# Kernel optimization log

Measured on AMD Instinct MI355X. Metric: run time of the kernel, lower is better.

## Reference

```python
import jax, jax.numpy as jnp
import numpy as np

D_MODEL = 1024
NUM_HEADS = 16
D_K = D_MODEL // NUM_HEADS


def setup_inputs() -> dict:
    key = jax.random.key(0)
    ks = jax.random.split(key, 11)
    B, S = 2, 2048
    scale = 1.0 / np.sqrt(D_MODEL)
    inp = {
        "Q": jax.random.normal(ks[0], (B, S, D_MODEL), jnp.float32),
        "K": jax.random.normal(ks[1], (B, S, D_MODEL), jnp.float32),
        "V": jax.random.normal(ks[2], (B, S, D_MODEL), jnp.float32),
        "W_q": jax.random.normal(ks[3], (D_MODEL, D_MODEL), jnp.float32) * scale,
        "b_q": jnp.zeros((D_MODEL,), jnp.float32),
        "W_k": jax.random.normal(ks[4], (D_MODEL, D_MODEL), jnp.float32) * scale,
        "b_k": jnp.zeros((D_MODEL,), jnp.float32),
        "W_v": jax.random.normal(ks[5], (D_MODEL, D_MODEL), jnp.float32) * scale,
        "b_v": jnp.zeros((D_MODEL,), jnp.float32),
        "W_o": jax.random.normal(ks[6], (D_MODEL, D_MODEL), jnp.float32) * scale,
        "b_o": jnp.zeros((D_MODEL,), jnp.float32),
    }
    return inp


def _split_heads(x):
    B, S, _ = x.shape
    return x.reshape(B, S, NUM_HEADS, D_K).transpose(0, 2, 1, 3)  # [B,H,S,dk]


def reference(Q, K, V, W_q, b_q, W_k, b_k, W_v, b_v, W_o, b_o):
    # Linear projections (torch Linear: x @ W^T + b)
    q = _split_heads(Q @ W_q.T + b_q)
    k = _split_heads(K @ W_k.T + b_k)
    v = _split_heads(V @ W_v.T + b_v)
    scale = 1.0 / jnp.sqrt(jnp.float32(D_K))
    scores = jnp.einsum("bhqd,bhkd->bhqk", q, k) * scale  # [B,H,S,S]
    attn = jax.nn.softmax(scores, axis=-1)
    # dropout is identity in eval mode
    out = jnp.einsum("bhqk,bhkd->bhqd", attn, v)  # [B,H,S,dk]
    B, H, S, dk = out.shape
    out = out.transpose(0, 2, 1, 3).reshape(B, S, H * dk)
    output = out @ W_o.T + b_o
    return output, attn
```

## Files before the change

### kernel.cpp

```cpp
#include <hip/hip_runtime.h>

typedef __bf16 bf16x8 __attribute__((ext_vector_type(8)));
typedef float f32x4 __attribute__((ext_vector_type(4)));
typedef unsigned short u16x4 __attribute__((ext_vector_type(4)));
typedef unsigned short u16x8 __attribute__((ext_vector_type(8)));

#define DEV __device__ __forceinline__

DEV unsigned short f2bf(float x) {
    union { float f; unsigned u; } v; v.f = x;
    unsigned r = (v.u + 0x7FFFu + ((v.u >> 16) & 1u)) >> 16;
    return (unsigned short)r;
}
DEV float bf2f(unsigned short h) {
    union { unsigned u; float f; } v; v.u = ((unsigned)h) << 16;
    return v.f;
}
DEV void gload16(const void* g, void* l) {
    __builtin_amdgcn_global_load_lds((const __attribute__((address_space(1))) void*)g,
                                     (__attribute__((address_space(3))) void*)l, 16, 0, 0);
}

__global__ __launch_bounds__(512) void gemm_proj(
    const float* __restrict__ A0, const float* __restrict__ A1, const float* __restrict__ A2,
    const float* __restrict__ W0, const float* __restrict__ W1, const float* __restrict__ W2,
    const float* __restrict__ B0, const float* __restrict__ B1, const float* __restrict__ B2,
    unsigned short* O0, unsigned short* O1, unsigned short* O2)
{
    const int raw = blockIdx.x;
    const int f = (raw & 7) * 48 + (raw >> 3);
    const int bx = f % 8;
    const int by = (f / 8) % 16;
    const int z  = f / 128;

    const float* A       = (z == 0) ? A0 : (z == 1) ? A1 : A2;
    const float* W       = (z == 0) ? W0 : (z == 1) ? W1 : W2;
    const float* bias    = (z == 0) ? B0 : (z == 1) ? B1 : B2;
    unsigned short* outp = (z == 0) ? O0 : (z == 1) ? O1 : O2;

    __shared__ unsigned short sA[256 * 32];
    __shared__ unsigned short sB[128 * 32];

    const int tid = threadIdx.x, lane = tid & 63;
    const int wv = tid >> 6, wrow = wv >> 2, wcol = wv & 3;
    const int l15 = lane & 15, lg = lane >> 4;
    const int row0 = by * 256, col0 = bx * 128;

    f32x4 acc[8][2];
#pragma unroll
    for (int m = 0; m < 8; ++m)
#pragma unroll
        for (int n = 0; n < 2; ++n) acc[m][n] = f32x4{0.f, 0.f, 0.f, 0.f};

    const int rA = tid >> 1, cA = (tid & 1) * 16;
    const int rB = tid >> 2, cB = (tid & 3) * 8;
    const float* Abase = A + (size_t)(row0 + rA) * 1024 + cA;
    const float* Wbase = W + (size_t)(col0 + rB) * 1024 + cB;

    for (int kt = 0; kt < 32; ++kt) {
        const int kf = kt * 32;
        f32x4 a0 = *(const f32x4*)(Abase + kf);
        f32x4 a1 = *(const f32x4*)(Abase + kf + 4);
        f32x4 a2 = *(const f32x4*)(Abase + kf + 8);
        f32x4 a3 = *(const f32x4*)(Abase + kf + 12);
        f32x4 w0 = *(const f32x4*)(Wbase + kf);
        f32x4 w1 = *(const f32x4*)(Wbase + kf + 4);
        u16x8 pa0, pa1, pw;
#pragma unroll
        for (int j = 0; j < 4; ++j) {
            pa0[j] = f2bf(a0[j]); pa0[4 + j] = f2bf(a1[j]);
            pa1[j] = f2bf(a2[j]); pa1[4 + j] = f2bf(a3[j]);
            pw[j]  = f2bf(w0[j]); pw[4 + j]  = f2bf(w1[j]);
        }
        __syncthreads();
        *(u16x8*)&sA[rA * 32 + cA]     = pa0;
        *(u16x8*)&sA[rA * 32 + cA + 8] = pa1;
        *(u16x8*)&sB[rB * 32 + cB]     = pw;
        __syncthreads();

        bf16x8 af[8], bfr[2];
#pragma unroll
        for (int m = 0; m < 8; ++m) {
            int arow = wrow * 128 + m * 16 + l15;
            af[m] = *(const bf16x8*)&sA[arow * 32 + lg * 8];
        }
#pragma unroll
        for (int n = 0; n < 2; ++n) {
            int bcol = wcol * 32 + n * 16 + l15;
            bfr[n] = *(const bf16x8*)&sB[bcol * 32 + lg * 8];
        }
#pragma unroll
        for (int m = 0; m < 8; ++m)
#pragma unroll
            for (int n = 0; n < 2; ++n)
                acc[m][n] = __builtin_amdgcn_mfma_f32_16x16x32_bf16(af[m], bfr[n], acc[m][n], 0, 0, 0);
    }

#pragma unroll
    for (int m = 0; m < 8; ++m) {
#pragma unroll
        for (int n = 0; n < 2; ++n) {
            const int C = col0 + wcol * 32 + n * 16 + l15;
            const int Rbase = row0 + wrow * 128 + m * 16 + lg * 4;
            const float bv = bias[C];
            const int bq = Rbase >> 11, s0 = Rbase & 2047, hh = C >> 6, dd = C & 63;
            if (z != 2) {
                const size_t base = ((size_t)(bq * 16 + hh) * 2048 + s0) * 64 + dd;
#pragma unroll
                for (int j = 0; j < 4; ++j)
                    outp[base + (size_t)j * 64] = f2bf(acc[m][n][j] + bv);
            } else {
                const size_t base = ((size_t)(bq * 16 + hh) * 64 + dd) * 2048 + s0;
                u16x4 pk;
#pragma unroll
                for (int j = 0; j < 4; ++j) pk[j] = f2bf(acc[m][n][j] + bv);
                *(u16x4*)&outp[base] = pk;
            }
        }
    }
}

__global__ __launch_bounds__(256) void gemm_final(
    const unsigned short* __restrict__ A, const float* __restrict__ W,
    const float* __restrict__ bias, float* __restrict__ out)
{
    const int raw = blockIdx.x;
    const int f = (raw & 7) * 64 + (raw >> 3);
    const int bx = f % 16;
    const int by = f / 16;

    __shared__ unsigned short sA[128 * 32];
    __shared__ unsigned short sB[64 * 32];

    const int tid = threadIdx.x, lane = tid & 63;
    const int wv = tid >> 6, wrow = wv >> 1, wcol = wv & 1;
    const int l15 = lane & 15, lg = lane >> 4;
    const int row0 = by * 128, col0 = bx * 64;

    f32x4 acc[4][2];
#pragma unroll
    for (int m = 0; m < 4; ++m)
#pragma unroll
        for (int n = 0; n < 2; ++n) acc[m][n] = f32x4{0.f, 0.f, 0.f, 0.f};

    const char* Ab = (const char*)(A + (size_t)row0 * 1024);
    const int o1 = tid * 16, o2 = (256 + tid) * 16;
    const int r1 = o1 >> 6, c1 = o1 & 63, r2 = o2 >> 6, c2 = o2 & 63;
    const int rB = tid >> 2, cB = (tid & 3) * 8;
    const float* Wbase = W + (size_t)(col0 + rB) * 1024 + cB;

    for (int kt = 0; kt < 32; ++kt) {
        const int kb = kt * 64;
        f32x4 w0 = *(const f32x4*)(Wbase + kt * 32);
        f32x4 w1 = *(const f32x4*)(Wbase + kt * 32 + 4);
        u16x8 pw;
#pragma unroll
        for (int j = 0; j < 4; ++j) { pw[j] = f2bf(w0[j]); pw[4 + j] = f2bf(w1[j]); }
        __syncthreads();
        gload16(Ab + (size_t)r1 * 2048 + kb + c1, (char*)sA + o1);
        gload16(Ab + (size_t)r2 * 2048 + kb + c2, (char*)sA + o2);
        *(u16x8*)&sB[rB * 32 + cB] = pw;
        __syncthreads();

        bf16x8 af[4], bfr[2];
#pragma unroll
        for (int m = 0; m < 4; ++m) {
            int arow = wrow * 64 + m * 16 + l15;
            af[m] = *(const bf16x8*)&sA[arow * 32 + lg * 8];
        }
#pragma unroll
        for (int n = 0; n < 2; ++n) {
            int bcol = wcol * 32 + n * 16 + l15;
            bfr[n] = *(const bf16x8*)&sB[bcol * 32 + lg * 8];
        }
#pragma unroll
        for (int m = 0; m < 4; ++m)
#pragma unroll
            for (int n = 0; n < 2; ++n)
                acc[m][n] = __builtin_amdgcn_mfma_f32_16x16x32_bf16(af[m], bfr[n], acc[m][n], 0, 0, 0);
    }

#pragma unroll
    for (int m = 0; m < 4; ++m) {
#pragma unroll
        for (int n = 0; n < 2; ++n) {
            const int C = col0 + wcol * 32 + n * 16 + l15;
            const int Rbase = row0 + wrow * 64 + m * 16 + lg * 4;
            const float bv = bias[C];
            const size_t base = (size_t)Rbase * 1024 + C;
#pragma unroll
            for (int j = 0; j < 4; ++j)
                __builtin_nontemporal_store(acc[m][n][j] + bv, &out[base + (size_t)j * 1024]);
        }
    }
}

__global__ __launch_bounds__(512, 1) void attn_k(
    const unsigned short* __restrict__ qh, const unsigned short* __restrict__ kh,
    const unsigned short* __restrict__ vT, unsigned short* __restrict__ oa,
    float* __restrict__ attn_out)
{
    __shared__ unsigned short p[32 * 2048];
    __shared__ float Olds[2][32][64];
    __shared__ float wsum[8][32];
    __shared__ float rinvw[8][32];

    const int tid = threadIdx.x, lane = tid & 63, w = tid >> 6;
    const int l15 = lane & 15, lg = lane >> 4;

    const int raw = blockIdx.x;
    const int f = (raw & 7) * 256 + (raw >> 3);
    const int q0 = (f & 63) * 32;
    const int h = (f >> 6) & 15, b = f >> 10;

    const size_t headoff = (size_t)(b * 16 + h) * 131072;
    const unsigned short* qhead = qh + headoff + (size_t)q0 * 64;
    const unsigned short* khead = kh + headoff;
    const unsigned short* vhead = vT + headoff;

    const int colbase = w * 256;
    const bf16x8 aq0 = *(const bf16x8*)(qhead + l15 * 64 + lg * 8);
    const bf16x8 aq1 = *(const bf16x8*)(qhead + l15 * 64 + 32 + lg * 8);
    const bf16x8 aq2 = *(const bf16x8*)(qhead + (16 + l15) * 64 + lg * 8);
    const bf16x8 aq3 = *(const bf16x8*)(qhead + (16 + l15) * 64 + 32 + lg * 8);

    const unsigned short* kptr = khead + (size_t)(colbase + l15) * 64 + lg * 8;
    bf16x8 kf0 = *(const bf16x8*)(kptr);
    bf16x8 kf1 = *(const bf16x8*)(kptr + 32);
    float psum0 = 0.f, psum1 = 0.f;

#pragma unroll
    for (int t = 0; t < 16; ++t) {
        bf16x8 nk0, nk1;
        if (t < 15) {
            const unsigned short* np = kptr + (size_t)(t + 1) * 1024;
            nk0 = *(const bf16x8*)(np);
            nk1 = *(const bf16x8*)(np + 32);
        }
        f32x4 c0 = {0.f, 0.f, 0.f, 0.f}, c1 = {0.f, 0.f, 0.f, 0.f};
        c0 = __builtin_amdgcn_mfma_f32_16x16x32_bf16(kf0, aq0, c0, 0, 0, 0);
        c1 = __builtin_amdgcn_mfma_f32_16x16x32_bf16(kf0, aq2, c1, 0, 0, 0);
        c0 = __builtin_amdgcn_mfma_f32_16x16x32_bf16(kf1, aq1, c0, 0, 0, 0);
        c1 = __builtin_amdgcn_mfma_f32_16x16x32_bf16(kf1, aq3, c1, 0, 0, 0);
        u16x4 pk0, pk1;
#pragma unroll
        for (int j = 0; j < 4; ++j) {
            float e0 = __expf(c0[j] * 0.125f);
            float e1 = __expf(c1[j] * 0.125f);
            psum0 += e0; psum1 += e1;
            pk0[j] = f2bf(e0); pk1[j] = f2bf(e1);
        }
        const int colb = (colbase + t * 16 + lg * 4) << 1;
        int b0 = (l15 << 12) + colb;         b0 ^= (l15 & 7) << 4;
        int b1 = ((16 + l15) << 12) + colb;  b1 ^= (l15 & 7) << 4;
        *(u16x4*)((char*)p + b0) = pk0;
        *(u16x4*)((char*)p + b1) = pk1;
        kf0 = nk0; kf1 = nk1;
    }

    psum0 += __shfl_xor(psum0, 16);
    psum0 += __shfl_xor(psum0, 32);
    psum1 += __shfl_xor(psum1, 16);
    psum1 += __shfl_xor(psum1, 32);
    if (lane < 16) {
        wsum[w][lane]      = psum0;
        wsum[w][16 + lane] = psum1;
    }
    __syncthreads();

    if (lane < 32) {
        float s = wsum[0][lane] + wsum[1][lane] + wsum[2][lane] + wsum[3][lane]
                + wsum[4][lane] + wsum[5][lane] + wsum[6][lane] + wsum[7][lane];
        rinvw[w][lane] = 1.0f / s;
    }

    float* aout = attn_out + ((size_t)(b * 16 + h) * 2048 + q0) * 2048;
    for (int i = 0; i < 32; ++i) {
        int byte = (i << 12) + (tid << 3);
        byte ^= (i & 7) << 4;
        const u16x4 pv = *(const u16x4*)((char*)p + byte);
        const float inv = rinvw[w][i];
        f32x4 ov = { bf2f(pv[0]) * inv, bf2f(pv[1]) * inv, bf2f(pv[2]) * inv, bf2f(pv[3]) * inv };
        __builtin_nontemporal_store(ov, (f32x4*)&aout[(size_t)i * 2048 + tid * 4]);
    }

    const int dq = w & 3, kh2 = w >> 2;
    const int d0 = dq * 16;
    f32x4 acc0 = {0.f, 0.f, 0.f, 0.f}, acc1 = {0.f, 0.f, 0.f, 0.f};
    const unsigned short* vptr = vhead + (size_t)(d0 + l15) * 2048 + kh2 * 1024 + lg * 8;
    bf16x8 vf = *(const bf16x8*)(vptr);
    for (int kc = 0; kc < 32; ++kc) {
        bf16x8 nvf;
        if (kc < 31) nvf = *(const bf16x8*)(vptr + (size_t)(kc + 1) * 32);
        const int colb = (kh2 * 1024 + kc * 32 + lg * 8) << 1;
        int b0 = (l15 << 12) + colb;         b0 ^= (l15 & 7) << 4;
        int b1 = ((16 + l15) << 12) + colb;  b1 ^= (l15 & 7) << 4;
        const bf16x8 pa0 = *(const bf16x8*)((char*)p + b0);
        const bf16x8 pa1 = *(const bf16x8*)((char*)p + b1);
        acc0 = __builtin_amdgcn_mfma_f32_16x16x32_bf16(pa0, vf, acc0, 0, 0, 0);
        acc1 = __builtin_amdgcn_mfma_f32_16x16x32_bf16(pa1, vf, acc1, 0, 0, 0);
        vf = nvf;
    }
#pragma unroll
    for (int j = 0; j < 4; ++j) {
        Olds[kh2][lg * 4 + j][d0 + l15]      = acc0[j];
        Olds[kh2][16 + lg * 4 + j][d0 + l15] = acc1[j];
    }
    __syncthreads();

    {
        const int q = tid >> 4, d4 = (tid & 15) * 4;
        f32x4 s = *(const f32x4*)&Olds[0][q][d4];
        s += *(const f32x4*)&Olds[1][q][d4];
        const float rq = rinvw[w][q];
        u16x4 pk;
#pragma unroll
        for (int j = 0; j < 4; ++j) pk[j] = f2bf(s[j] * rq);
        *(u16x4*)&oa[((size_t)b * 2048 + q0 + q) * 1024 + h * 64 + d4] = pk;
    }
}

extern "C" void kernel_launch(void* const* d_in, const int* in_sizes, int n_in,
                              void* d_out, int out_size, void* d_ws, size_t ws_size,
                              hipStream_t stream) {
    const float* Q  = (const float*)d_in[0];
    const float* K  = (const float*)d_in[1];
    const float* V  = (const float*)d_in[2];
    const float* Wq = (const float*)d_in[3];
    const float* bq = (const float*)d_in[4];
    const float* Wk = (const float*)d_in[5];
    const float* bk = (const float*)d_in[6];
    const float* Wv = (const float*)d_in[7];
    const float* bv = (const float*)d_in[8];
    const float* Wo = (const float*)d_in[9];
    const float* bo = (const float*)d_in[10];

    char* ws = (char*)d_ws;
    unsigned short* qhd = (unsigned short*)(ws + 33554432);
    unsigned short* khd = (unsigned short*)(ws + 41943040);
    unsigned short* vTd = (unsigned short*)(ws + 50331648);
    unsigned short* oad = (unsigned short*)(ws + 58720256);

    float* out = (float*)d_out;
    float* attn_out = out + 4194304;

    gemm_proj<<<dim3(384), 512, 0, stream>>>(Q, K, V, Wq, Wk, Wv,
                                             bq, bk, bv, qhd, khd, vTd);

    attn_k<<<dim3(2048), 512, 0, stream>>>(qhd, khd, vTd, oad, attn_out);

    gemm_final<<<dim3(512), 256, 0, stream>>>(oad, Wo, bo, out);
}
```

Measured before the change: 249.7 us.

## Fuse P·V into the score loop using register-held probabilities and permuted V layout

The projection kernel now writes transposed V with a permuted sequence order, so the bf16 probability fragments produced by the QK^T MFMAs can be fed directly as A operands of the P·V MFMAs without going back through LDS. Each wave accumulates its own partial output over its 256 key columns, and the partials from all 8 waves are reduced through LDS, reusing the probability buffer. This removes the separate P·V pass that re-read P from LDS and overlaps the V loads with the score computation. The costs are more registers, an 8-way instead of 2-way reduction, and an extra barrier; launch bounds were also changed to ask for 2 blocks per CU, though 128KB of shared memory probably still limits occupancy to one.

```diff
diff --git a/kernel.cpp b/kernel.cpp
--- a/kernel.cpp
+++ b/kernel.cpp
@@ -110,7 +110,8 @@
                 for (int j = 0; j < 4; ++j)
                     outp[base + (size_t)j * 64] = f2bf(acc[m][n][j] + bv);
             } else {
-                const size_t base = ((size_t)(bq * 16 + hh) * 64 + dd) * 2048 + s0;
+                const int sp = (s0 & ~31) + (((s0 >> 2) & 3) << 3) + (((s0 >> 4) & 1) << 2);
+                const size_t base = ((size_t)(bq * 16 + hh) * 64 + dd) * 2048 + sp;
                 u16x4 pk;
 #pragma unroll
                 for (int j = 0; j < 4; ++j) pk[j] = f2bf(acc[m][n][j] + bv);
@@ -195,13 +196,12 @@
     }
 }
 
-__global__ __launch_bounds__(512, 1) void attn_k(
+__global__ __launch_bounds__(512, 2) void attn_k(
     const unsigned short* __restrict__ qh, const unsigned short* __restrict__ kh,
     const unsigned short* __restrict__ vT, unsigned short* __restrict__ oa,
     float* __restrict__ attn_out)
 {
     __shared__ unsigned short p[32 * 2048];
-    __shared__ float Olds[2][32][64];
     __shared__ float wsum[8][32];
     __shared__ float rinvw[8][32];
 
@@ -225,9 +225,23 @@
     const bf16x8 aq3 = *(const bf16x8*)(qhead + (16 + l15) * 64 + 32 + lg * 8);
 
     const unsigned short* kptr = khead + (size_t)(colbase + l15) * 64 + lg * 8;
+    const unsigned short* vbase = vhead + (size_t)l15 * 2048 + colbase + lg * 8;
+
     bf16x8 kf0 = *(const bf16x8*)(kptr);
     bf16x8 kf1 = *(const bf16x8*)(kptr + 32);
+    bf16x8 vfc[4], vfn[4];
+#pragma unroll
+    for (int dq = 0; dq < 4; ++dq)
+        vfc[dq] = *(const bf16x8*)(vbase + (size_t)dq * 32768);
+
     float psum0 = 0.f, psum1 = 0.f;
+    f32x4 oacc[2][4];
+#pragma unroll
+    for (int qh2 = 0; qh2 < 2; ++qh2)
+#pragma unroll
+        for (int dq = 0; dq < 4; ++dq) oacc[qh2][dq] = f32x4{0.f, 0.f, 0.f, 0.f};
+
+    u16x4 pe0, pe1;
 
 #pragma unroll
     for (int t = 0; t < 16; ++t) {
@@ -237,6 +251,12 @@
             nk0 = *(const bf16x8*)(np);
             nk1 = *(const bf16x8*)(np + 32);
         }
+        if ((t & 1) == 0 && t < 14) {
+            const int nc = (t >> 1) + 1;
+#pragma unroll
+            for (int dq = 0; dq < 4; ++dq)
+                vfn[dq] = *(const bf16x8*)(vbase + (size_t)dq * 32768 + nc * 32);
+        }
         f32x4 c0 = {0.f, 0.f, 0.f, 0.f}, c1 = {0.f, 0.f, 0.f, 0.f};
         c0 = __builtin_amdgcn_mfma_f32_16x16x32_bf16(kf0, aq0, c0, 0, 0, 0);
         c1 = __builtin_amdgcn_mfma_f32_16x16x32_bf16(kf0, aq2, c1, 0, 0, 0);
@@ -250,11 +270,32 @@
             psum0 += e0; psum1 += e1;
             pk0[j] = f2bf(e0); pk1[j] = f2bf(e1);
         }
-        const int colb = (colbase + t * 16 + lg * 4) << 1;
-        int b0 = (l15 << 12) + colb;         b0 ^= (l15 & 7) << 4;
-        int b1 = ((16 + l15) << 12) + colb;  b1 ^= (l15 & 7) << 4;
-        *(u16x4*)((char*)p + b0) = pk0;
-        *(u16x4*)((char*)p + b1) = pk1;
+        {
+            const int colb = (colbase + t * 16 + lg * 4) << 1;
+            int b0 = (l15 << 12) + colb;         b0 ^= (l15 & 7) << 4;
+            int b1 = ((16 + l15) << 12) + colb;  b1 ^= (l15 & 7) << 4;
+            *(u16x4*)((char*)p + b0) = pk0;
+            *(u16x4*)((char*)p + b1) = pk1;
+        }
+        if ((t & 1) == 0) {
+            pe0 = pk0; pe1 = pk1;
+        } else {
+            u16x8 a0v, a1v;
+#pragma unroll
+            for (int j = 0; j < 4; ++j) {
+                a0v[j] = pe0[j]; a0v[4 + j] = pk0[j];
+                a1v[j] = pe1[j]; a1v[4 + j] = pk1[j];
+            }
+            const bf16x8 a0 = __builtin_bit_cast(bf16x8, a0v);
+            const bf16x8 a1 = __builtin_bit_cast(bf16x8, a1v);
+#pragma unroll
+            for (int dq = 0; dq < 4; ++dq) {
+                oacc[0][dq] = __builtin_amdgcn_mfma_f32_16x16x32_bf16(a0, vfc[dq], oacc[0][dq], 0, 0, 0);
+                oacc[1][dq] = __builtin_amdgcn_mfma_f32_16x16x32_bf16(a1, vfc[dq], oacc[1][dq], 0, 0, 0);
+            }
+#pragma unroll
+            for (int dq = 0; dq < 4; ++dq) vfc[dq] = vfn[dq];
+        }
         kf0 = nk0; kf1 = nk1;
     }
 
@@ -283,35 +324,24 @@
         f32x4 ov = { bf2f(pv[0]) * inv, bf2f(pv[1]) * inv, bf2f(pv[2]) * inv, bf2f(pv[3]) * inv };
         __builtin_nontemporal_store(ov, (f32x4*)&aout[(size_t)i * 2048 + tid * 4]);
     }
-
-    const int dq = w & 3, kh2 = w >> 2;
-    const int d0 = dq * 16;
-    f32x4 acc0 = {0.f, 0.f, 0.f, 0.f}, acc1 = {0.f, 0.f, 0.f, 0.f};
-    const unsigned short* vptr = vhead + (size_t)(d0 + l15) * 2048 + kh2 * 1024 + lg * 8;
-    bf16x8 vf = *(const bf16x8*)(vptr);
-    for (int kc = 0; kc < 32; ++kc) {
-        bf16x8 nvf;
-        if (kc < 31) nvf = *(const bf16x8*)(vptr + (size_t)(kc + 1) * 32);
-        const int colb = (kh2 * 1024 + kc * 32 + lg * 8) << 1;
-        int b0 = (l15 << 12) + colb;         b0 ^= (l15 & 7) << 4;
-        int b1 = ((16 + l15) << 12) + colb;  b1 ^= (l15 & 7) << 4;
-        const bf16x8 pa0 = *(const bf16x8*)((char*)p + b0);
-        const bf16x8 pa1 = *(const bf16x8*)((char*)p + b1);
-        acc0 = __builtin_amdgcn_mfma_f32_16x16x32_bf16(pa0, vf, acc0, 0, 0, 0);
-        acc1 = __builtin_amdgcn_mfma_f32_16x16x32_bf16(pa1, vf, acc1, 0, 0, 0);
-        vf = nvf;
-    }
-#pragma unroll
-    for (int j = 0; j < 4; ++j) {
-        Olds[kh2][lg * 4 + j][d0 + l15]      = acc0[j];
-        Olds[kh2][16 + lg * 4 + j][d0 + l15] = acc1[j];
-    }
+    __syncthreads();
+
+    float* olds = (float*)p;
+#pragma unroll
+    for (int qh2 = 0; qh2 < 2; ++qh2)
+#pragma unroll
+        for (int dq = 0; dq < 4; ++dq)
+#pragma unroll
+            for (int j = 0; j < 4; ++j)
+                olds[w * 2048 + (qh2 * 16 + lg * 4 + j) * 64 + dq * 16 + l15] = oacc[qh2][dq][j];
     __syncthreads();
 
     {
         const int q = tid >> 4, d4 = (tid & 15) * 4;
-        f32x4 s = *(const f32x4*)&Olds[0][q][d4];
-        s += *(const f32x4*)&Olds[1][q][d4];
+        f32x4 s = *(const f32x4*)&olds[q * 64 + d4];
+#pragma unroll
+        for (int w2 = 1; w2 < 8; ++w2)
+            s += *(const f32x4*)&olds[w2 * 2048 + q * 64 + d4];
         const float rq = rinvw[w][q];
         u16x4 pk;
 #pragma unroll
```

Result: slower. 262.8 us (+5.2%).
